# Performance work log

Measured on AMD Instinct MI355X. Metric: run time of the kernel, lower is better.

Reference implementation:

```python
import jax, jax.numpy as jnp
import numpy as np

N_NODES = 100000


def _gcn_conv(x, W, b, src, dst, n):
    # PyG GCNConv: h = x @ W; add self-loops; norm = d^-1/2[src] * d^-1/2[dst];
    # out[i] = sum_{(s->i)} norm * h[s] + b
    h = x @ W  # [N, F_out]
    deg = jax.ops.segment_sum(jnp.ones_like(dst, dtype=h.dtype), dst, num_segments=n)
    dis = jnp.where(deg > 0, jax.lax.rsqrt(jnp.maximum(deg, 1.0)), 0.0)
    norm = dis[src] * dis[dst]  # [E]
    msg = h[src] * norm[:, None]  # [E, F_out] gather + scale
    out = jax.ops.segment_sum(msg, dst, num_segments=n)  # scatter-add
    return out + b


def _add_self_loops(edge_index, n):
    loops = jnp.arange(n, dtype=edge_index.dtype)
    src = jnp.concatenate([edge_index[0], loops])
    dst = jnp.concatenate([edge_index[1], loops])
    return src, dst


def setup_inputs() -> dict:
    key = jax.random.key(0)
    k_x, k_e, k_w1, k_w2 = jax.random.split(key, 4)
    n, e, f_in, f_hid = N_NODES, 1600000, 128, 64
    x = jax.random.normal(k_x, (n, f_in), dtype=jnp.float32)
    edge_index = jax.random.randint(k_e, (2, e), 0, n, dtype=jnp.int64)
    # Glorot-ish init for weights
    W1 = jax.random.normal(k_w1, (f_in, f_hid), dtype=jnp.float32) / np.sqrt(f_in)
    b1 = jnp.zeros((f_hid,), dtype=jnp.float32)
    W2 = jax.random.normal(k_w2, (f_hid, f_hid), dtype=jnp.float32) / np.sqrt(f_hid)
    b2 = jnp.zeros((f_hid,), dtype=jnp.float32)
    return {"x": x, "edge_index": edge_index, "W1": W1, "b1": b1, "W2": W2, "b2": b2}


def reference(x, edge_index, W1, b1, W2, b2):
    n = x.shape[0]
    src, dst = _add_self_loops(edge_index, n)
    h = jax.nn.relu(_gcn_conv(x, W1, b1, src, dst, n))
    # F.dropout(training=False) in eval mode is identity
    out = _gcn_conv(h, W2, b2, src, dst, n)
    return out
```

## Files before the change

### kernel.cpp

```cpp
#include <hip/hip_runtime.h>
#include <hip/hip_bf16.h>


#define FOUT 64
#define BW 128
#define BSH 7
#define MAXB 1024
#define CHUNK 4096
#define SLAB 3072

#define NT1 1024
#define NT2 512

__device__ __forceinline__ float bf2f(unsigned int u16) {
    union { unsigned int i; float f; } c;
    c.i = u16 << 16;
    return c.f;
}
__device__ __forceinline__ unsigned short f2bf(float f) {
    union { float f; unsigned int i; } c;
    c.f = f;
    unsigned int i = c.i;
    return (unsigned short)((i + 0x7FFFu + ((i >> 16) & 1u)) >> 16);
}

typedef __attribute__((ext_vector_type(8))) short short8v;
typedef __attribute__((ext_vector_type(4))) float f32x4;

__device__ __forceinline__ void split_frag(const float* xa, short8v* Ah, short8v* Al) {
    union { unsigned int u[4]; short8v v; } H, L;
#pragma unroll
    for (int p = 0; p < 4; p++) {
        unsigned short h0 = f2bf(xa[2 * p]);
        unsigned short h1 = f2bf(xa[2 * p + 1]);
        H.u[p] = (unsigned int)h0 | ((unsigned int)h1 << 16);
        unsigned short l0 = f2bf(xa[2 * p] - bf2f(h0));
        unsigned short l1 = f2bf(xa[2 * p + 1] - bf2f(h1));
        L.u[p] = (unsigned int)l0 | ((unsigned int)l1 << 16);
    }
    *Ah = H.v;
    *Al = L.v;
}

__device__ __forceinline__ void conv_w_frag(const float* __restrict__ W,
                                            unsigned short* __restrict__ WhF,
                                            unsigned short* __restrict__ WlF,
                                            int task) {
    const int lane = task & 63;
    const int cf = (task >> 6) & 3;
    const int s = task >> 8;
    const int q = lane >> 4, m = lane & 15;
#pragma unroll
    for (int j = 0; j < 8; j++) {
        int k = s * 32 + q * 8 + j;
        float x = W[(size_t)k * 64 + cf * 16 + m];
        unsigned short h = f2bf(x);
        WhF[(size_t)task * 8 + j] = h;
        WlF[(size_t)task * 8 + j] = f2bf(x - bf2f(h));
    }
}

__global__ __launch_bounds__(512) void edge_hist(
    const int* __restrict__ dst, int* __restrict__ cnt, int E,
    const float* __restrict__ W1, const float* __restrict__ W2,
    unsigned short* __restrict__ whf1, unsigned short* __restrict__ wlf1,
    unsigned short* __restrict__ whf2, unsigned short* __restrict__ wlf2) {
    __shared__ int h[MAXB];
    const int blk = blockIdx.x, t = threadIdx.x;
    h[t] = 0;
    h[t + 512] = 0;
    __syncthreads();
    const int e0 = blk * CHUNK;
#pragma unroll
    for (int k = 0; k < CHUNK / 512; k++) {
        int e = e0 + k * 512 + t;
        if (e < E) atomicAdd(&h[dst[e] >> BSH], 1);
    }
    if (blk == 0) {
        for (int task = t; task < NT1 + NT2; task += 512) {
            if (task < NT1) conv_w_frag(W1, whf1, wlf1, task);
            else            conv_w_frag(W2, whf2, wlf2, task - NT1);
        }
    }
    __syncthreads();
    cnt[blk * MAXB + t] = h[t];
    cnt[blk * MAXB + t + 512] = h[t + 512];
}

__global__ __launch_bounds__(512) void col_scan(int* __restrict__ cnt, int nblk,
                                                int* __restrict__ gcnt) {
    __shared__ int ts[512];
    const int b = blockIdx.x;
    const int t = threadIdx.x;
    int v = (t < nblk) ? cnt[t * MAXB + b] : 0;
    ts[t] = v;
    __syncthreads();
    for (int off = 1; off < 512; off <<= 1) {
        int x = (t >= off) ? ts[t - off] : 0;
        __syncthreads();
        ts[t] += x;
        __syncthreads();
    }
    if (t < nblk) cnt[t * MAXB + b] = b * SLAB + ts[t] - v;
    if (t == 511) gcnt[b] = ts[511];
}

__global__ __launch_bounds__(512) void edge_place(
    const int* __restrict__ src, const int* __restrict__ dst,
    const int* __restrict__ cnt, int* __restrict__ ebuf, int E) {
    __shared__ int lbase[MAXB];
    __shared__ int cur[MAXB];
    const int blk = blockIdx.x, t = threadIdx.x;
    lbase[t] = cnt[blk * MAXB + t];
    lbase[t + 512] = cnt[blk * MAXB + t + 512];
    cur[t] = 0;
    cur[t + 512] = 0;
    __syncthreads();
    const int e0 = blk * CHUNK;
#pragma unroll
    for (int k = 0; k < CHUNK / 512; k++) {
        int e = e0 + k * 512 + t;
        if (e < E) {
            int d = dst[e];
            int b = d >> BSH;
            int r = atomicAdd(&cur[b], 1);
            ebuf[lbase[b] + r] = src[e] | ((d & (BW - 1)) << 17);
        }
    }
}

template <int K>
__global__ __launch_bounds__(256) void csr_gemm(
    int* __restrict__ ebuf, const int* __restrict__ gcnt,
    unsigned int* __restrict__ rowinfo, float* __restrict__ dis, int n,
    const float* __restrict__ X, const unsigned short* __restrict__ WhF,
    const unsigned short* __restrict__ WlF, unsigned short* __restrict__ HS) {
    __shared__ int ldeg[BW];
    __shared__ float sdis[BW];
    __shared__ int wtot[2];
    const int b = blockIdx.x, t = threadIdx.x;
    const int node0 = b << BSH;
    const int nn = min(BW, n - node0);
    const int ebeg = b * SLAB;

    int raw[SLAB / 256];
#pragma unroll
    for (int k = 0; k < SLAB / 256; k++) raw[k] = ebuf[ebeg + t + k * 256];

    const int cnt = gcnt[b];
    if (t < BW) ldeg[t] = 0;
    __syncthreads();

    int w[SLAB / 256];
#pragma unroll
    for (int k = 0; k < SLAB / 256; k++) {
        w[k] = (t + k * 256 < cnt) ? raw[k] : -1;
        if (w[k] >= 0) atomicAdd(&ldeg[w[k] >> 17], 1);
    }
    __syncthreads();

    int v = 0, pv = 0;
    if (t < BW) { v = ldeg[t]; pv = v; }
#pragma unroll
    for (int d = 1; d < 64; d <<= 1) {
        int x = __shfl_up(pv, d);
        if ((t & 63) >= d) pv += x;
    }
    if (t < BW && (t & 63) == 63) wtot[t >> 6] = pv;
    __syncthreads();
    if (t < BW && t >= 64) pv += wtot[0];
    const int ex = pv - v;
    if (t < nn) {
        rowinfo[node0 + t] = ((unsigned int)(ebeg + ex) << 8) | (unsigned int)v;
        float dv = rsqrtf((float)v + 1.0f);
        dis[node0 + t] = dv;
        sdis[t] = dv;
    } else if (t < BW) {
        sdis[t] = 0.f;
    }
    if (t < BW) ldeg[t] = ex;
    __syncthreads();
#pragma unroll
    for (int k = 0; k < SLAB / 256; k++)
        if (w[k] >= 0) {
            int r = atomicAdd(&ldeg[w[k] >> 17], 1);
            ebuf[ebeg + r] = w[k] & 0x1FFFF;
        }

    const int lane = t & 63;
    const int wvv = t >> 6;
    const int m = lane & 15;
    const int q = lane >> 4;
#pragma unroll 1
    for (int t2 = 0; t2 < 2; t2++) {
        const int tile = wvv * 2 + t2;
        const int wrow0 = node0 + tile * 16;
        f32x4 acc[4];
#pragma unroll
        for (int cf = 0; cf < 4; cf++) acc[cf] = (f32x4)0.f;

        const int arow = wrow0 + m;
        const bool rok = (arow < n);
        const float* xp = X + (size_t)arow * K + q * 8;
#pragma unroll
        for (int s = 0; s < K / 32; s++) {
            float4 v0, v1;
            if (rok) {
                v0 = *(const float4*)(xp + s * 32);
                v1 = *(const float4*)(xp + s * 32 + 4);
            } else {
                v0 = make_float4(0.f, 0.f, 0.f, 0.f);
                v1 = v0;
            }
            const float xa[8] = {v0.x, v0.y, v0.z, v0.w, v1.x, v1.y, v1.z, v1.w};
            short8v Ah, Al;
            split_frag(xa, &Ah, &Al);
            const unsigned short* wh = WhF + ((size_t)(s * 4) * 64 + lane) * 8;
            const unsigned short* wl = WlF + ((size_t)(s * 4) * 64 + lane) * 8;
#pragma unroll
            for (int cf = 0; cf < 4; cf++) {
                short8v bh = *(const short8v*)(wh + (size_t)cf * 64 * 8);
                short8v bl = *(const short8v*)(wl + (size_t)cf * 64 * 8);
                acc[cf] = __builtin_amdgcn_mfma_f32_16x16x32_bf16(Ah, bh, acc[cf], 0, 0, 0);
                acc[cf] = __builtin_amdgcn_mfma_f32_16x16x32_bf16(Al, bh, acc[cf], 0, 0, 0);
                acc[cf] = __builtin_amdgcn_mfma_f32_16x16x32_bf16(Ah, bl, acc[cf], 0, 0, 0);
            }
        }
#pragma unroll
        for (int r = 0; r < 4; r++) {
            int row = wrow0 + q * 4 + r;
            if (row < n) {
                float dr = sdis[tile * 16 + q * 4 + r];
#pragma unroll
                for (int cf = 0; cf < 4; cf++) {
                    HS[(size_t)row * FOUT + cf * 16 + m] = f2bf(acc[cf][r] * dr);
                }
            }
        }
    }
}

__device__ __forceinline__ void acc8(const uint4 u, float* a) {
    a[0] += bf2f(u.x & 0xFFFFu); a[1] += bf2f(u.x >> 16);
    a[2] += bf2f(u.y & 0xFFFFu); a[3] += bf2f(u.y >> 16);
    a[4] += bf2f(u.z & 0xFFFFu); a[5] += bf2f(u.z >> 16);
    a[6] += bf2f(u.w & 0xFFFFu); a[7] += bf2f(u.w >> 16);
}

#define OSTR 68
__global__ __launch_bounds__(256) void agg_gemm(
    const uint4* __restrict__ hsv, const unsigned int* __restrict__ rowinfo,
    const int* __restrict__ col, const float* __restrict__ dis,
    const float* __restrict__ bias,
    const unsigned short* __restrict__ WhF2, const unsigned short* __restrict__ WlF2,
    unsigned short* __restrict__ HS2, int n) {
    __shared__ float so[32 * OSTR];
    const int tid = threadIdx.x;
    const int wv = tid >> 6;
    const int lane = tid & 63;
    const int g = lane >> 3;
    const int jj = lane & 7;
    const int lrow = wv * 8 + g;
    const int i = blockIdx.x * 32 + lrow;

    float o[8];
#pragma unroll
    for (int p = 0; p < 8; p++) o[p] = 0.f;

    if (i < n) {
        const unsigned int info = rowinfo[i];
        const int beg = (int)(info >> 8);
        const int end = beg + (int)(info & 255u);

        float a[8];
        {
            uint4 su = hsv[(size_t)i * 8 + jj];
            a[0] = bf2f(su.x & 0xFFFFu); a[1] = bf2f(su.x >> 16);
            a[2] = bf2f(su.y & 0xFFFFu); a[3] = bf2f(su.y >> 16);
            a[4] = bf2f(su.z & 0xFFFFu); a[5] = bf2f(su.z >> 16);
            a[6] = bf2f(su.w & 0xFFFFu); a[7] = bf2f(su.w >> 16);
        }
        const int gb = g << 3;
        for (int chunk = beg; chunk < end; chunk += 8) {
            int m = end - chunk;
            if (m > 8) m = 8;
            int c = (chunk + jj < end) ? col[chunk + jj] : 0;
            int q = 0;
            for (; q + 4 <= m; q += 4) {
                int s0 = __shfl(c, gb + q);
                int s1 = __shfl(c, gb + q + 1);
                int s2 = __shfl(c, gb + q + 2);
                int s3 = __shfl(c, gb + q + 3);
                uint4 u0 = hsv[(size_t)s0 * 8 + jj];
                uint4 u1 = hsv[(size_t)s1 * 8 + jj];
                uint4 u2 = hsv[(size_t)s2 * 8 + jj];
                uint4 u3 = hsv[(size_t)s3 * 8 + jj];
                acc8(u0, a);
                acc8(u1, a);
                acc8(u2, a);
                acc8(u3, a);
            }
            for (; q < m; q++) {
                int s = __shfl(c, gb + q);
                acc8(hsv[(size_t)s * 8 + jj], a);
            }
        }
        float d = dis[i];
        const float4* b4 = (const float4*)bias;
        float4 bb0 = b4[jj * 2];
        float4 bb1 = b4[jj * 2 + 1];
        o[0] = fmaxf(d * a[0] + bb0.x, 0.f);
        o[1] = fmaxf(d * a[1] + bb0.y, 0.f);
        o[2] = fmaxf(d * a[2] + bb0.z, 0.f);
        o[3] = fmaxf(d * a[3] + bb0.w, 0.f);
        o[4] = fmaxf(d * a[4] + bb1.x, 0.f);
        o[5] = fmaxf(d * a[5] + bb1.y, 0.f);
        o[6] = fmaxf(d * a[6] + bb1.z, 0.f);
        o[7] = fmaxf(d * a[7] + bb1.w, 0.f);
    }
    {
        float* sp = &so[lrow * OSTR + jj * 8];
        *(float4*)sp = make_float4(o[0], o[1], o[2], o[3]);
        *(float4*)(sp + 4) = make_float4(o[4], o[5], o[6], o[7]);
    }
    __syncthreads();

    const int tile = wv >> 1;
    const int ch = wv & 1;
    const int m = lane & 15;
    const int q = lane >> 4;
    f32x4 acc[2];
    acc[0] = (f32x4)0.f;
    acc[1] = (f32x4)0.f;
#pragma unroll
    for (int s = 0; s < 2; s++) {
        const float* ap = &so[(tile * 16 + m) * OSTR + s * 32 + q * 8];
        float4 v0 = *(const float4*)ap;
        float4 v1 = *(const float4*)(ap + 4);
        const float xa[8] = {v0.x, v0.y, v0.z, v0.w, v1.x, v1.y, v1.z, v1.w};
        short8v Ah, Al;
        split_frag(xa, &Ah, &Al);
#pragma unroll
        for (int c = 0; c < 2; c++) {
            int cf = ch * 2 + c;
            const unsigned short* wh = WhF2 + ((size_t)(s * 4 + cf) * 64 + lane) * 8;
            const unsigned short* wl = WlF2 + ((size_t)(s * 4 + cf) * 64 + lane) * 8;
            short8v bh = *(const short8v*)wh;
            short8v bl = *(const short8v*)wl;
            acc[c] = __builtin_amdgcn_mfma_f32_16x16x32_bf16(Ah, bh, acc[c], 0, 0, 0);
            acc[c] = __builtin_amdgcn_mfma_f32_16x16x32_bf16(Al, bh, acc[c], 0, 0, 0);
            acc[c] = __builtin_amdgcn_mfma_f32_16x16x32_bf16(Ah, bl, acc[c], 0, 0, 0);
        }
    }
#pragma unroll
    for (int r = 0; r < 4; r++) {
        int lr = tile * 16 + q * 4 + r;
        int i2 = blockIdx.x * 32 + lr;
        if (i2 < n) {
            float dr = dis[i2];
#pragma unroll
            for (int c = 0; c < 2; c++) {
                HS2[(size_t)i2 * FOUT + (ch * 2 + c) * 16 + m] = f2bf(acc[c][r] * dr);
            }
        }
    }
}

template <bool RELU>
__global__ __launch_bounds__(256) void aggregate(
    const uint4* __restrict__ hsv, const unsigned int* __restrict__ rowinfo,
    const int* __restrict__ col, const float* __restrict__ dis,
    const float* __restrict__ bias, float* __restrict__ out, int n) {
    const int wave = blockIdx.x * 4 + (threadIdx.x >> 6);
    const int lane = threadIdx.x & 63;
    const int g  = lane >> 3;
    const int jj = lane & 7;
    const int i = wave * 8 + g;
    if (i >= n) return;

    const unsigned int info = rowinfo[i];
    const int beg = (int)(info >> 8);
    const int end = beg + (int)(info & 255u);

    float a[8];
    {
        uint4 su = hsv[(size_t)i * 8 + jj];
        a[0] = bf2f(su.x & 0xFFFFu); a[1] = bf2f(su.x >> 16);
        a[2] = bf2f(su.y & 0xFFFFu); a[3] = bf2f(su.y >> 16);
        a[4] = bf2f(su.z & 0xFFFFu); a[5] = bf2f(su.z >> 16);
        a[6] = bf2f(su.w & 0xFFFFu); a[7] = bf2f(su.w >> 16);
    }

    const int gb = g << 3;
    for (int chunk = beg; chunk < end; chunk += 8) {
        int m = end - chunk;
        if (m > 8) m = 8;
        int c = (chunk + jj < end) ? col[chunk + jj] : 0;
        int q = 0;
        for (; q + 4 <= m; q += 4) {
            int s0 = __shfl(c, gb + q);
            int s1 = __shfl(c, gb + q + 1);
            int s2 = __shfl(c, gb + q + 2);
            int s3 = __shfl(c, gb + q + 3);
            uint4 u0 = hsv[(size_t)s0 * 8 + jj];
            uint4 u1 = hsv[(size_t)s1 * 8 + jj];
            uint4 u2 = hsv[(size_t)s2 * 8 + jj];
            uint4 u3 = hsv[(size_t)s3 * 8 + jj];
            acc8(u0, a);
            acc8(u1, a);
            acc8(u2, a);
            acc8(u3, a);
        }
        for (; q < m; q++) {
            int s = __shfl(c, gb + q);
            acc8(hsv[(size_t)s * 8 + jj], a);
        }
    }
    float d = dis[i];
    const float4* b4 = (const float4*)bias;
    float4 bb0 = b4[jj * 2];
    float4 bb1 = b4[jj * 2 + 1];
    float4 o0, o1;
    o0.x = d * a[0] + bb0.x; o0.y = d * a[1] + bb0.y;
    o0.z = d * a[2] + bb0.z; o0.w = d * a[3] + bb0.w;
    o1.x = d * a[4] + bb1.x; o1.y = d * a[5] + bb1.y;
    o1.z = d * a[6] + bb1.z; o1.w = d * a[7] + bb1.w;
    if (RELU) {
        o0.x = fmaxf(o0.x, 0.f); o0.y = fmaxf(o0.y, 0.f);
        o0.z = fmaxf(o0.z, 0.f); o0.w = fmaxf(o0.w, 0.f);
        o1.x = fmaxf(o1.x, 0.f); o1.y = fmaxf(o1.y, 0.f);
        o1.z = fmaxf(o1.z, 0.f); o1.w = fmaxf(o1.w, 0.f);
    }
    float4* orow = (float4*)out + (size_t)i * 16 + jj * 2;
    orow[0] = o0;
    orow[1] = o1;
}

extern "C" void kernel_launch(void* const* d_in, const int* in_sizes, int n_in,
                              void* d_out, int out_size, void* d_ws, size_t ws_size,
                              hipStream_t stream) {
    const float* x  = (const float*)d_in[0];
    const int*   ei = (const int*)d_in[1];
    const float* W1 = (const float*)d_in[2];
    const float* b1 = (const float*)d_in[3];
    const float* W2 = (const float*)d_in[4];
    const float* b2 = (const float*)d_in[5];

    const int n = in_sizes[0] / 128;
    const int E = in_sizes[1] / 2;
    const int* srcp = ei;
    const int* dstp = ei + E;

    float* out = (float*)d_out;

    const int B = (n + BW - 1) / BW;
    const int nblk = (E + CHUNK - 1) / CHUNK;

    int*            cnt     = (int*)d_ws;
    int*            gcnt    = cnt + 512 * MAXB;
    unsigned int*   rowinfo = (unsigned int*)(gcnt + MAXB);
    float*          dis     = (float*)(rowinfo + n);
    int*            ebuf    = (int*)(dis + n);
    unsigned short* hs      = (unsigned short*)(ebuf + (size_t)B * SLAB);
    unsigned short* whf1    = hs + (size_t)n * FOUT;
    unsigned short* wlf1    = whf1 + (size_t)NT1 * 8;
    unsigned short* whf2    = wlf1 + (size_t)NT1 * 8;
    unsigned short* wlf2    = whf2 + (size_t)NT2 * 8;
    unsigned short* hs2     = wlf2 + (size_t)NT2 * 8;

    edge_hist<<<nblk, 512, 0, stream>>>(dstp, cnt, E, W1, W2,
                                        whf1, wlf1, whf2, wlf2);
    col_scan<<<B, 512, 0, stream>>>(cnt, nblk, gcnt);
    edge_place<<<nblk, 512, 0, stream>>>(srcp, dstp, cnt, ebuf, E);

    csr_gemm<128><<<B, 256, 0, stream>>>(ebuf, gcnt, rowinfo, dis, n,
                                         x, whf1, wlf1, hs);

    agg_gemm<<<(n + 31) / 32, 256, 0, stream>>>(
        (const uint4*)hs, rowinfo, ebuf, dis, b1, whf2, wlf2, hs2, n);

    aggregate<false><<<(n + 31) / 32, 256, 0, stream>>>(
        (const uint4*)hs2, rowinfo, ebuf, dis, b2, out, n);
}
```

Baseline: 224.3 us.

## Stage CSR column indices in LDS and software-pipeline X loads in csr_gemm

The two aggregation kernels now copy each block's contiguous span of column indices into shared memory with a cooperative load. Each row's neighbours are then read from LDS instead of through per-chunk global loads and shuffles, falling back to global reads if the span exceeds the buffer. The self-row load is issued before the staging barrier. In csr_gemm, both 16-row tiles per wave are processed together, and the first X fragment is prefetched before the edge sort, with the next step's X loads issued ahead of the current MFMAs to overlap memory latency. This raises register pressure, and the aggregation kernels gain an extra block-wide barrier and 8KB of LDS each.

Measured after the change: 217.5 us. 1.03x faster.

```diff
diff --git a/kernel.cpp b/kernel.cpp
--- a/kernel.cpp
+++ b/kernel.cpp
@@ -11,6 +11,7 @@
 
 #define NT1 1024
 #define NT2 512
+#define LCOLN 2048
 
 __device__ __forceinline__ float bf2f(unsigned int u16) {
     union { unsigned int i; float f; } c;
@@ -129,12 +130,12 @@
     }
 }
 
-template <int K>
 __global__ __launch_bounds__(256) void csr_gemm(
     int* __restrict__ ebuf, const int* __restrict__ gcnt,
     unsigned int* __restrict__ rowinfo, float* __restrict__ dis, int n,
     const float* __restrict__ X, const unsigned short* __restrict__ WhF,
     const unsigned short* __restrict__ WlF, unsigned short* __restrict__ HS) {
+    constexpr int K = 128;
     __shared__ int ldeg[BW];
     __shared__ float sdis[BW];
     __shared__ int wtot[2];
@@ -143,6 +144,22 @@
     const int nn = min(BW, n - node0);
     const int ebeg = b * SLAB;
 
+    const int lane = t & 63;
+    const int wvv = t >> 6;
+    const int m = lane & 15;
+    const int q = lane >> 4;
+    const int tile0 = wvv * 2, tile1 = wvv * 2 + 1;
+    const int r0 = node0 + tile0 * 16 + m;
+    const int r1 = node0 + tile1 * 16 + m;
+    const bool ok0 = (r0 < n), ok1 = (r1 < n);
+    const float* xp0 = X + (size_t)r0 * K + q * 8;
+    const float* xp1 = X + (size_t)r1 * K + q * 8;
+    const float4 zf4 = make_float4(0.f, 0.f, 0.f, 0.f);
+
+    float4 c00 = zf4, c01 = zf4, c10 = zf4, c11 = zf4;
+    if (ok0) { c00 = *(const float4*)xp0; c01 = *(const float4*)(xp0 + 4); }
+    if (ok1) { c10 = *(const float4*)xp1; c11 = *(const float4*)(xp1 + 4); }
+
     int raw[SLAB / 256];
 #pragma unroll
     for (int k = 0; k < SLAB / 256; k++) raw[k] = ebuf[ebeg + t + k * 256];
@@ -164,9 +181,9 @@
 #pragma unroll
     for (int d = 1; d < 64; d <<= 1) {
         int x = __shfl_up(pv, d);
-        if ((t & 63) >= d) pv += x;
-    }
-    if (t < BW && (t & 63) == 63) wtot[t >> 6] = pv;
+        if ((lane) >= d) pv += x;
+    }
+    if (t < BW && lane == 63) wtot[t >> 6] = pv;
     __syncthreads();
     if (t < BW && t >= 64) pv += wtot[0];
     const int ex = pv - v;
@@ -187,55 +204,67 @@
             ebuf[ebeg + r] = w[k] & 0x1FFFF;
         }
 
-    const int lane = t & 63;
-    const int wvv = t >> 6;
-    const int m = lane & 15;
-    const int q = lane >> 4;
-#pragma unroll 1
-    for (int t2 = 0; t2 < 2; t2++) {
-        const int tile = wvv * 2 + t2;
-        const int wrow0 = node0 + tile * 16;
-        f32x4 acc[4];
-#pragma unroll
-        for (int cf = 0; cf < 4; cf++) acc[cf] = (f32x4)0.f;
-
-        const int arow = wrow0 + m;
-        const bool rok = (arow < n);
-        const float* xp = X + (size_t)arow * K + q * 8;
-#pragma unroll
-        for (int s = 0; s < K / 32; s++) {
-            float4 v0, v1;
-            if (rok) {
-                v0 = *(const float4*)(xp + s * 32);
-                v1 = *(const float4*)(xp + s * 32 + 4);
-            } else {
-                v0 = make_float4(0.f, 0.f, 0.f, 0.f);
-                v1 = v0;
-            }
-            const float xa[8] = {v0.x, v0.y, v0.z, v0.w, v1.x, v1.y, v1.z, v1.w};
-            short8v Ah, Al;
-            split_frag(xa, &Ah, &Al);
-            const unsigned short* wh = WhF + ((size_t)(s * 4) * 64 + lane) * 8;
-            const unsigned short* wl = WlF + ((size_t)(s * 4) * 64 + lane) * 8;
-#pragma unroll
-            for (int cf = 0; cf < 4; cf++) {
-                short8v bh = *(const short8v*)(wh + (size_t)cf * 64 * 8);
-                short8v bl = *(const short8v*)(wl + (size_t)cf * 64 * 8);
-                acc[cf] = __builtin_amdgcn_mfma_f32_16x16x32_bf16(Ah, bh, acc[cf], 0, 0, 0);
-                acc[cf] = __builtin_amdgcn_mfma_f32_16x16x32_bf16(Al, bh, acc[cf], 0, 0, 0);
-                acc[cf] = __builtin_amdgcn_mfma_f32_16x16x32_bf16(Ah, bl, acc[cf], 0, 0, 0);
-            }
-        }
-#pragma unroll
-        for (int r = 0; r < 4; r++) {
-            int row = wrow0 + q * 4 + r;
-            if (row < n) {
-                float dr = sdis[tile * 16 + q * 4 + r];
-#pragma unroll
-                for (int cf = 0; cf < 4; cf++) {
-                    HS[(size_t)row * FOUT + cf * 16 + m] = f2bf(acc[cf][r] * dr);
-                }
-            }
+    f32x4 acc0[4], acc1[4];
+#pragma unroll
+    for (int cf = 0; cf < 4; cf++) { acc0[cf] = (f32x4)0.f; acc1[cf] = (f32x4)0.f; }
+    float4 n00, n01, n10, n11;
+
+#define GSTEP(S)                                                                        \
+    {                                                                                   \
+        if ((S) + 1 < K / 32) {                                                         \
+            n00 = zf4; n01 = zf4; n10 = zf4; n11 = zf4;                                 \
+            if (ok0) { n00 = *(const float4*)(xp0 + ((S) + 1) * 32);                    \
+                       n01 = *(const float4*)(xp0 + ((S) + 1) * 32 + 4); }              \
+            if (ok1) { n10 = *(const float4*)(xp1 + ((S) + 1) * 32);                    \
+                       n11 = *(const float4*)(xp1 + ((S) + 1) * 32 + 4); }              \
+        }                                                                               \
+        const unsigned short* wh = WhF + ((size_t)((S) * 4) * 64 + lane) * 8;           \
+        const unsigned short* wl = WlF + ((size_t)((S) * 4) * 64 + lane) * 8;           \
+        short8v Ah, Al;                                                                 \
+        {                                                                               \
+            const float xa[8] = {c00.x, c00.y, c00.z, c00.w, c01.x, c01.y, c01.z, c01.w}; \
+            split_frag(xa, &Ah, &Al);                                                   \
+        }                                                                               \
+        _Pragma("unroll")                                                               \
+        for (int cf = 0; cf < 4; cf++) {                                                \
+            short8v bh = *(const short8v*)(wh + (size_t)cf * 64 * 8);                   \
+            short8v bl = *(const short8v*)(wl + (size_t)cf * 64 * 8);                   \
+            acc0[cf] = __builtin_amdgcn_mfma_f32_16x16x32_bf16(Ah, bh, acc0[cf], 0, 0, 0); \
+            acc0[cf] = __builtin_amdgcn_mfma_f32_16x16x32_bf16(Al, bh, acc0[cf], 0, 0, 0); \
+            acc0[cf] = __builtin_amdgcn_mfma_f32_16x16x32_bf16(Ah, bl, acc0[cf], 0, 0, 0); \
+        }                                                                               \
+        {                                                                               \
+            const float xa[8] = {c10.x, c10.y, c10.z, c10.w, c11.x, c11.y, c11.z, c11.w}; \
+            split_frag(xa, &Ah, &Al);                                                   \
+        }                                                                               \
+        _Pragma("unroll")                                                               \
+        for (int cf = 0; cf < 4; cf++) {                                                \
+            short8v bh = *(const short8v*)(wh + (size_t)cf * 64 * 8);                   \
+            short8v bl = *(const short8v*)(wl + (size_t)cf * 64 * 8);                   \
+            acc1[cf] = __builtin_amdgcn_mfma_f32_16x16x32_bf16(Ah, bh, acc1[cf], 0, 0, 0); \
+            acc1[cf] = __builtin_amdgcn_mfma_f32_16x16x32_bf16(Al, bh, acc1[cf], 0, 0, 0); \
+            acc1[cf] = __builtin_amdgcn_mfma_f32_16x16x32_bf16(Ah, bl, acc1[cf], 0, 0, 0); \
+        }                                                                               \
+        c00 = n00; c01 = n01; c10 = n10; c11 = n11;                                     \
+    }
+    GSTEP(0) GSTEP(1) GSTEP(2) GSTEP(3)
+#undef GSTEP
+
+#pragma unroll
+    for (int r = 0; r < 4; r++) {
+        int row = node0 + tile0 * 16 + q * 4 + r;
+        if (row < n) {
+            float dr = sdis[tile0 * 16 + q * 4 + r];
+#pragma unroll
+            for (int cf = 0; cf < 4; cf++)
+                HS[(size_t)row * FOUT + cf * 16 + m] = f2bf(acc0[cf][r] * dr);
+        }
+        row = node0 + tile1 * 16 + q * 4 + r;
+        if (row < n) {
+            float dr = sdis[tile1 * 16 + q * 4 + r];
+#pragma unroll
+            for (int cf = 0; cf < 4; cf++)
+                HS[(size_t)row * FOUT + cf * 16 + m] = f2bf(acc1[cf][r] * dr);
         }
     }
 }
@@ -245,6 +274,26 @@
     a[2] += bf2f(u.y & 0xFFFFu); a[3] += bf2f(u.y >> 16);
     a[4] += bf2f(u.z & 0xFFFFu); a[5] += bf2f(u.z >> 16);
     a[6] += bf2f(u.w & 0xFFFFu); a[7] += bf2f(u.w >> 16);
+}
+
+__device__ __forceinline__ void stage_cols(
+    const unsigned int* __restrict__ rowinfo, const int* __restrict__ col,
+    int* lcol, int* sbs, int i0, int n, int tid) {
+    if (tid == 0) {
+        int last = min(i0 + 31, n - 1);
+        unsigned int r0 = rowinfo[i0];
+        unsigned int rl = rowinfo[last];
+        int base = (int)(r0 >> 8);
+        sbs[0] = base;
+        sbs[1] = (int)(rl >> 8) + (int)(rl & 255u) - base;
+    }
+    __syncthreads();
+    const int span = sbs[1];
+    if (span <= LCOLN) {
+        const int base = sbs[0];
+        for (int k = tid; k < span; k += 256) lcol[k] = col[base + k];
+    }
+    __syncthreads();
 }
 
 #define OSTR 68
@@ -255,55 +304,55 @@
     const unsigned short* __restrict__ WhF2, const unsigned short* __restrict__ WlF2,
     unsigned short* __restrict__ HS2, int n) {
     __shared__ float so[32 * OSTR];
+    __shared__ int lcol[LCOLN];
+    __shared__ int sbs[2];
     const int tid = threadIdx.x;
     const int wv = tid >> 6;
     const int lane = tid & 63;
     const int g = lane >> 3;
     const int jj = lane & 7;
     const int lrow = wv * 8 + g;
-    const int i = blockIdx.x * 32 + lrow;
+    const int i0 = blockIdx.x * 32;
+    const int i = i0 + lrow;
+
+    const unsigned int info = (i < n) ? rowinfo[i] : 0u;
+    uint4 su = make_uint4(0u, 0u, 0u, 0u);
+    if (i < n) su = hsv[(size_t)i * 8 + jj];
+
+    stage_cols(rowinfo, col, lcol, sbs, i0, n, tid);
+    const int base = sbs[0], span = sbs[1];
+    const bool uselds = (span <= LCOLN);
 
     float o[8];
 #pragma unroll
     for (int p = 0; p < 8; p++) o[p] = 0.f;
 
     if (i < n) {
-        const unsigned int info = rowinfo[i];
         const int beg = (int)(info >> 8);
-        const int end = beg + (int)(info & 255u);
+        const int deg = (int)(info & 255u);
+        const int off = beg - base;
 
         float a[8];
-        {
-            uint4 su = hsv[(size_t)i * 8 + jj];
-            a[0] = bf2f(su.x & 0xFFFFu); a[1] = bf2f(su.x >> 16);
-            a[2] = bf2f(su.y & 0xFFFFu); a[3] = bf2f(su.y >> 16);
-            a[4] = bf2f(su.z & 0xFFFFu); a[5] = bf2f(su.z >> 16);
-            a[6] = bf2f(su.w & 0xFFFFu); a[7] = bf2f(su.w >> 16);
-        }
-        const int gb = g << 3;
-        for (int chunk = beg; chunk < end; chunk += 8) {
-            int m = end - chunk;
-            if (m > 8) m = 8;
-            int c = (chunk + jj < end) ? col[chunk + jj] : 0;
-            int q = 0;
-            for (; q + 4 <= m; q += 4) {
-                int s0 = __shfl(c, gb + q);
-                int s1 = __shfl(c, gb + q + 1);
-                int s2 = __shfl(c, gb + q + 2);
-                int s3 = __shfl(c, gb + q + 3);
-                uint4 u0 = hsv[(size_t)s0 * 8 + jj];
-                uint4 u1 = hsv[(size_t)s1 * 8 + jj];
-                uint4 u2 = hsv[(size_t)s2 * 8 + jj];
-                uint4 u3 = hsv[(size_t)s3 * 8 + jj];
-                acc8(u0, a);
-                acc8(u1, a);
-                acc8(u2, a);
-                acc8(u3, a);
-            }
-            for (; q < m; q++) {
-                int s = __shfl(c, gb + q);
-                acc8(hsv[(size_t)s * 8 + jj], a);
-            }
+        a[0] = bf2f(su.x & 0xFFFFu); a[1] = bf2f(su.x >> 16);
+        a[2] = bf2f(su.y & 0xFFFFu); a[3] = bf2f(su.y >> 16);
+        a[4] = bf2f(su.z & 0xFFFFu); a[5] = bf2f(su.z >> 16);
+        a[6] = bf2f(su.w & 0xFFFFu); a[7] = bf2f(su.w >> 16);
+
+        int qq = 0;
+        for (; qq + 4 <= deg; qq += 4) {
+            int s0 = uselds ? lcol[off + qq]     : col[beg + qq];
+            int s1 = uselds ? lcol[off + qq + 1] : col[beg + qq + 1];
+            int s2 = uselds ? lcol[off + qq + 2] : col[beg + qq + 2];
+            int s3 = uselds ? lcol[off + qq + 3] : col[beg + qq + 3];
+            uint4 u0 = hsv[(size_t)s0 * 8 + jj];
+            uint4 u1 = hsv[(size_t)s1 * 8 + jj];
+            uint4 u2 = hsv[(size_t)s2 * 8 + jj];
+            uint4 u3 = hsv[(size_t)s3 * 8 + jj];
+            acc8(u0, a); acc8(u1, a); acc8(u2, a); acc8(u3, a);
+        }
+        for (; qq < deg; qq++) {
+            int s = uselds ? lcol[off + qq] : col[beg + qq];
+            acc8(hsv[(size_t)s * 8 + jj], a);
         }
         float d = dis[i];
         const float4* b4 = (const float4*)bias;
@@ -371,50 +420,51 @@
     const uint4* __restrict__ hsv, const unsigned int* __restrict__ rowinfo,
     const int* __restrict__ col, const float* __restrict__ dis,
     const float* __restrict__ bias, float* __restrict__ out, int n) {
-    const int wave = blockIdx.x * 4 + (threadIdx.x >> 6);
-    const int lane = threadIdx.x & 63;
-    const int g  = lane >> 3;
+    __shared__ int lcol[LCOLN];
+    __shared__ int sbs[2];
+    const int tid = threadIdx.x;
+    const int wv = tid >> 6;
+    const int lane = tid & 63;
+    const int g = lane >> 3;
     const int jj = lane & 7;
-    const int i = wave * 8 + g;
+    const int i0 = blockIdx.x * 32;
+    const int i = i0 + wv * 8 + g;
+
+    const unsigned int info = (i < n) ? rowinfo[i] : 0u;
+    uint4 su = make_uint4(0u, 0u, 0u, 0u);
+    if (i < n) su = hsv[(size_t)i * 8 + jj];
+
+    stage_cols(rowinfo, col, lcol, sbs, i0, n, tid);
+    const int base = sbs[0], span = sbs[1];
+    const bool uselds = (span <= LCOLN);
+
     if (i >= n) return;
 
-    const unsigned int info = rowinfo[i];
     const int beg = (int)(info >> 8);
-    const int end = beg + (int)(info & 255u);
+    const int deg = (int)(info & 255u);
+    const int off = beg - base;
 
     float a[8];
-    {
-        uint4 su = hsv[(size_t)i * 8 + jj];
-        a[0] = bf2f(su.x & 0xFFFFu); a[1] = bf2f(su.x >> 16);
-        a[2] = bf2f(su.y & 0xFFFFu); a[3] = bf2f(su.y >> 16);
-        a[4] = bf2f(su.z & 0xFFFFu); a[5] = bf2f(su.z >> 16);
-        a[6] = bf2f(su.w & 0xFFFFu); a[7] = bf2f(su.w >> 16);
-    }
-
-    const int gb = g << 3;
-    for (int chunk = beg; chunk < end; chunk += 8) {
-        int m = end - chunk;
-        if (m > 8) m = 8;
-        int c = (chunk + jj < end) ? col[chunk + jj] : 0;
-        int q = 0;
-        for (; q + 4 <= m; q += 4) {
-            int s0 = __shfl(c, gb + q);
-            int s1 = __shfl(c, gb + q + 1);
-            int s2 = __shfl(c, gb + q + 2);
-            int s3 = __shfl(c, gb + q + 3);
-            uint4 u0 = hsv[(size_t)s0 * 8 + jj];
-            uint4 u1 = hsv[(size_t)s1 * 8 + jj];
-            uint4 u2 = hsv[(size_t)s2 * 8 + jj];
-            uint4 u3 = hsv[(size_t)s3 * 8 + jj];
-            acc8(u0, a);
-            acc8(u1, a);
-            acc8(u2, a);
-            acc8(u3, a);
-        }
-        for (; q < m; q++) {
-            int s = __shfl(c, gb + q);
-            acc8(hsv[(size_t)s * 8 + jj], a);
-        }
+    a[0] = bf2f(su.x & 0xFFFFu); a[1] = bf2f(su.x >> 16);
+    a[2] = bf2f(su.y & 0xFFFFu); a[3] = bf2f(su.y >> 16);
+    a[4] = bf2f(su.z & 0xFFFFu); a[5] = bf2f(su.z >> 16);
+    a[6] = bf2f(su.w & 0xFFFFu); a[7] = bf2f(su.w >> 16);
+
+    int qq = 0;
+    for (; qq + 4 <= deg; qq += 4) {
+        int s0 = uselds ? lcol[off + qq]     : col[beg + qq];
+        int s1 = uselds ? lcol[off + qq + 1] : col[beg + qq + 1];
+        int s2 = uselds ? lcol[off + qq + 2] : col[beg + qq + 2];
+        int s3 = uselds ? lcol[off + qq + 3] : col[beg + qq + 3];
+        uint4 u0 = hsv[(size_t)s0 * 8 + jj];
+        uint4 u1 = hsv[(size_t)s1 * 8 + jj];
+        uint4 u2 = hsv[(size_t)s2 * 8 + jj];
+        uint4 u3 = hsv[(size_t)s3 * 8 + jj];
+        acc8(u0, a); acc8(u1, a); acc8(u2, a); acc8(u3, a);
+    }
+    for (; qq < deg; qq++) {
+        int s = uselds ? lcol[off + qq] : col[beg + qq];
+        acc8(hsv[(size_t)s * 8 + jj], a);
     }
     float d = dis[i];
     const float4* b4 = (const float4*)bias;
@@ -473,8 +523,8 @@
     col_scan<<<B, 512, 0, stream>>>(cnt, nblk, gcnt);
     edge_place<<<nblk, 512, 0, stream>>>(srcp, dstp, cnt, ebuf, E);
 
-    csr_gemm<128><<<B, 256, 0, stream>>>(ebuf, gcnt, rowinfo, dis, n,
-                                         x, whf1, wlf1, hs);
+    csr_gemm<<<B, 256, 0, stream>>>(ebuf, gcnt, rowinfo, dis, n,
+                                    x, whf1, wlf1, hs);
 
     agg_gemm<<<(n + 31) / 32, 256, 0, stream>>>(
         (const uint4*)hs, rowinfo, ebuf, dis, b1, whf2, wlf2, hs2, n);
```
